# Performance work log

Measured on AMD Instinct MI355X. Metric: run time of the kernel, lower is better.

The kernel has to match this reference:

```python
import jax, jax.numpy as jnp
import numpy as np

N = 256  # n_neurons
S = 32   # state_dim
M = 32   # message_dim
E = 32   # edge_dim
B = 64   # batch
N_IN = 16

def setup_inputs() -> dict:
    key = jax.random.key(0)
    ks = jax.random.split(key, 12)
    sc = 0.1
    return {
        "inputs": jax.random.normal(ks[0], (B, N_IN, S), jnp.float32),
        "initial_state": jax.random.normal(ks[1], (N, S), jnp.float32) * sc,
        "edge_matrix": jax.random.normal(ks[2], (N, N, E), jnp.float32) * sc,
        "Wf": jax.random.normal(ks[3], (E, M * S), jnp.float32) * sc,
        "bf": jnp.zeros((M * S,), jnp.float32),
        "Wz": jax.random.normal(ks[4], (M, S), jnp.float32) * sc,
        "Uz": jax.random.normal(ks[5], (S, S), jnp.float32) * sc,
        "bz": jnp.zeros((S,), jnp.float32),
        "Wr": jax.random.normal(ks[6], (M, S), jnp.float32) * sc,
        "Ur": jax.random.normal(ks[7], (S, S), jnp.float32) * sc,
        "br": jnp.zeros((S,), jnp.float32),
        "Wh": jax.random.normal(ks[8], (M, S), jnp.float32) * sc,
        "Uh": jax.random.normal(ks[9], (S, S), jnp.float32) * sc,
        "bh": jnp.zeros((S,), jnp.float32),
        "n_outputs": 16,
    }

def reference(inputs, initial_state, edge_matrix, Wf, bf, Wz, Uz, bz, Wr, Ur, br, Wh, Uh, bh, n_outputs):
    b, n_in, s = inputs.shape
    n = initial_state.shape[0]
    # filter generation: [N,N,E] -> [N,N,M,S]
    filters = (edge_matrix @ Wf + bf).reshape(n, n, M, s)
    # init + scatter inputs into hidden state (neuron i <- inputs[:, i, :])
    h = jnp.tile(initial_state[None], (b, 1, 1)).at[:, :n_in, :].set(inputs)
    # dense edge-filtered message passing: messages[b,j,m] = sum_i filters[i,j,m,s] h[b,i,s]
    messages = jnp.einsum('bis,ijms->bjm', h, filters)
    # GRU update with message as input
    z = jax.nn.sigmoid(messages @ Wz + h @ Uz + bz)
    r = jax.nn.sigmoid(messages @ Wr + h @ Ur + br)
    h_tilde = jnp.tanh(messages @ Wh + (r * h) @ Uh + bh)
    h_new = (1.0 - z) * h + z * h_tilde
    # gather outputs from the last n_outputs neurons (reversed), permute to [n_out, B, S]
    out_idx = n - 1 - jnp.arange(n_outputs)
    outputs = jnp.transpose(h_new[:, out_idx, :], (1, 0, 2))
    return (outputs, h_new)
```

## Files before the change

### kernel.cpp

```cpp
#include <hip/hip_runtime.h>

typedef unsigned short u16;
typedef __attribute__((ext_vector_type(4))) unsigned short u16x4;
typedef __attribute__((ext_vector_type(8))) unsigned short u16x8;
typedef __attribute__((ext_vector_type(4))) float f32x4;


__device__ __forceinline__ u16 f2bf(float x){
  unsigned u = __builtin_bit_cast(unsigned, x);
  u += 0x7FFFu + ((u >> 16) & 1u);
  return (u16)(u >> 16);
}
__device__ __forceinline__ void mfma1616(f32x4& acc, u16x8 a, u16x8 b){
  asm volatile("v_mfma_f32_16x16x32_bf16 %0, %1, %2, %0" : "+v"(acc) : "v"(a), "v"(b));
}
__device__ __forceinline__ void gl16(const void* g, void* l){
  __builtin_amdgcn_global_load_lds((const __attribute__((address_space(1))) void*)g,
                                   (__attribute__((address_space(3))) void*)l, 16, 0, 0);
}
__device__ __forceinline__ float sigm(float x){ return 1.f/(1.f + __expf(-x)); }
__device__ __forceinline__ float tanh_f(float x){ return 1.f - 2.f/(1.f + __expf(2.f*x)); }

__global__ __launch_bounds__(256) void k_prep(const float* __restrict__ inputs, const float* __restrict__ init,
    const float* __restrict__ EM, const float* __restrict__ Wf, const float* __restrict__ bfv,
    const float* __restrict__ Wz, const float* __restrict__ Uz, const float* __restrict__ Wr,
    const float* __restrict__ Ur, const float* __restrict__ Wh, const float* __restrict__ Uh,
    u16* __restrict__ hT, u16* __restrict__ EMT, u16* __restrict__ Wf5,
    float* __restrict__ bterm, u16* __restrict__ wsT){
  __shared__ float tl[64*65];
  const int bid = blockIdx.x, t = threadIdx.x;
  if (bid < 512){
    int bx = bid & 127, by = bid >> 7;
    int i0 = by*64, c0 = bx*64;
#pragma unroll
    for (int p=0;p<4;++p){
      int ri = p*16 + (t>>4), c4 = (t&15)*4;
      f32x4 v = *(const f32x4*)(EM + (i0+ri)*8192 + c0 + c4);
#pragma unroll
      for (int q=0;q<4;++q) tl[ri*65 + c4 + q] = v[q];
    }
    __syncthreads();
#pragma unroll
    for (int p=0;p<4;++p){
      int rc = p*16 + (t>>4), i4 = (t&15)*4;
      u16x4 o;
#pragma unroll
      for (int q=0;q<4;++q) o[q] = f2bf(tl[(i4+q)*65 + rc]);
      *(u16x4*)(EMT + (c0+rc)*256 + i0 + i4) = o;
    }
  } else if (bid < 1024){
    int base = ((bid-512)*256 + t)*4;
    int r = base >> 8, i0 = base & 255;
    int b = r >> 5, s = r & 31;
    u16x4 v;
#pragma unroll
    for (int q=0;q<4;++q){
      int i = i0 + q;
      float x = (i < 16) ? inputs[(b*16 + i)*32 + s] : init[i*32 + s];
      v[q] = f2bf(x);
    }
    *(u16x4*)(hT + base) = v;
  } else if (bid < 1056){
    int o = ((bid-1024)*256 + t)*4;
    int m = o >> 10, rem = o & 1023, s = rem >> 5, e0 = rem & 31;
    u16x4 v;
#pragma unroll
    for (int q=0;q<4;++q) v[q] = f2bf(Wf[(e0+q)*1024 + m*32 + s]);
    *(u16x4*)(Wf5 + o) = v;
  } else if (bid < 1120){
    int b = bid - 1056;
    float* red = tl;
    float* hsum = tl + 256;
    int g = t >> 5, s = t & 31;
    float acc = 0.f;
    for (int c=0;c<32;++c){
      int i = c*8 + g;
      acc += (i < 16) ? inputs[(b*16 + i)*32 + s] : init[i*32 + s];
    }
    red[g*32 + s] = acc;
    __syncthreads();
    if (t < 32){
      float v = 0.f;
#pragma unroll
      for (int gg=0;gg<8;++gg) v += red[gg*32 + t];
      hsum[t] = v;
    }
    __syncthreads();
    if (t < 32){
      float v = 0.f;
      for (int s2=0;s2<32;++s2) v += hsum[s2] * bfv[t*32 + s2];
      bterm[b*32 + t] = v;
    }
  } else {
    const float* Ws[6] = {Wz,Uz,Wr,Ur,Wh,Uh};
    for (int idx = t; idx < 6144; idx += 256){
      int g = idx >> 10, r2 = idx & 1023, s = r2 >> 5, k = r2 & 31;
      wsT[g*1024 + s*32 + k] = f2bf(Ws[g][k*32 + s]);
    }
  }
}

__global__ __launch_bounds__(256, 3) void k_mega(const u16* __restrict__ hT, const u16* __restrict__ EMT,
    const u16* __restrict__ Wf5, const float* __restrict__ bterm, const u16* __restrict__ wsT,
    const float* __restrict__ inputs, const float* __restrict__ init,
    const float* __restrict__ bz, const float* __restrict__ br, const float* __restrict__ bh,
    float* __restrict__ out){
  __shared__ char smem[48128];
  const int t = threadIdx.x, w = t >> 6, l = t & 63;
  const int rb = blockIdx.x & 15, cb = blockIdx.x >> 4;
  const int r0 = rb*128, c0 = cb*128;
  const int wrow = (w >> 1)*64, wcol = (w & 1)*64;

  f32x4 acc[4][4];
#pragma unroll
  for (int i=0;i<4;++i)
#pragma unroll
    for (int j=0;j<4;++j)
#pragma unroll
      for (int q=0;q<4;++q) acc[i][j][q] = 0.f;

  for (int st=0; st<4; ++st){
    const int kk = st*64;
#pragma unroll
    for (int p=0;p<4;++p){
      int q = p*256 + t, r = q>>3, sl = q&7;
      gl16(hT + (r0 + r)*256 + kk + ((sl ^ (r&7))*8), smem + q*16);
    }
#pragma unroll
    for (int p=0;p<4;++p){
      int q = p*256 + t, c = q>>3, sl = q&7;
      gl16(EMT + (c0 + c)*256 + kk + ((sl ^ (c&7))*8), smem + 16384 + q*16);
    }
    __syncthreads();
#pragma unroll
    for (int ks=0; ks<2; ++ks){
      const int kg = ks*4 + (l>>4);
      u16x8 af[4], bfr[4];
#pragma unroll
      for (int mf=0; mf<4; ++mf){
        int row = wrow + mf*16 + (l&15);
        af[mf] = *(const u16x8*)(smem + row*128 + ((kg ^ (row&7))<<4));
      }
#pragma unroll
      for (int nf=0; nf<4; ++nf){
        int col = wcol + nf*16 + (l&15);
        bfr[nf] = *(const u16x8*)(smem + 16384 + col*128 + ((kg ^ (col&7))<<4));
      }
#pragma unroll
      for (int mf=0; mf<4; ++mf)
#pragma unroll
        for (int nf=0; nf<4; ++nf)
          mfma1616(acc[mf][nf], af[mf], bfr[nf]);
    }
    __syncthreads();
  }

#pragma unroll
  for (int mf=0;mf<4;++mf)
#pragma unroll
    for (int nf=0;nf<4;++nf){
      int colg = wcol + nf*16 + (l&15);
#pragma unroll
      for (int q=0;q<4;++q){
        int rowg = wrow + mf*16 + (l>>4)*4 + q;
        *(u16*)(smem + rowg*256 + ((colg*2) ^ ((rowg&7)<<4))) = f2bf(acc[mf][nf][q]);
      }
    }
  __syncthreads();

  f32x4 ea0, ea1;
#pragma unroll
  for (int q=0;q<4;++q){ ea0[q]=0.f; ea1[q]=0.f; }
  {
    const int colbj = l & 15;
    const int bloc = colbj >> 2, jloc = colbj & 3;
    const int eg = (l >> 4)*8;
#pragma unroll
    for (int ss=0; ss<8; ++ss){
      int s = w*8 + ss;
      int row = bloc*32 + s;
      u16x8 bfr = *(const u16x8*)(smem + row*256 + ((jloc*64 + eg*2) ^ ((row&7)<<4)));
      u16x8 af0 = *(const u16x8*)(Wf5 + colbj*1024 + s*32 + eg);
      u16x8 af1 = *(const u16x8*)(Wf5 + (16+colbj)*1024 + s*32 + eg);
      mfma1616(ea0, af0, bfr);
      mfma1616(ea1, af1, bfr);
    }
  }
  float* red = (float*)(smem + 32768);
  *(f32x4*)(red + ((w*2+0)*64 + l)*4) = ea0;
  *(f32x4*)(red + ((w*2+1)*64 + l)*4) = ea1;
  __syncthreads();

  float* Lmsg = (float*)(smem + 40960);
  u16*   Lmsgb = (u16*)(smem + 43008);
  float* Lh   = (float*)(smem + 44032);
  u16*   Lhb  = (u16*)(smem + 46080);
  u16*   Lrh  = (u16*)(smem + 47104);
  for (int o = t; o < 512; o += 256){
    int row = o >> 5, m = o & 31;
    int hh = m >> 4, mloc = m & 15;
    int lsrc = row | ((mloc >> 2) << 4);
    int q = mloc & 3;
    float sum = 0.f;
#pragma unroll
    for (int wv=0; wv<4; ++wv) sum += red[((wv*2+hh)*64 + lsrc)*4 + q];
    int bg = rb*4 + (row>>2), jg = cb*4 + (row&3);
    float mval = sum + bterm[bg*32 + m];
    Lmsg[row*32+m] = mval; Lmsgb[row*32+m] = f2bf(mval);
    float hval = (jg < 16) ? inputs[(bg*16 + jg)*32 + m] : init[jg*32 + m];
    Lh[row*32+m] = hval; Lhb[row*32+m] = f2bf(hval);
  }
  __syncthreads();

  if (w == 0){
    const int rloc = l & 15;
    const int kg8 = (l >> 4)*8;
    u16x8 am = *(const u16x8*)(Lmsgb + rloc*32 + kg8);
    u16x8 ah = *(const u16x8*)(Lhb   + rloc*32 + kg8);
    u16x8 wz0 = *(const u16x8*)(wsT + 0*1024 + rloc*32 + kg8);
    u16x8 wz1 = *(const u16x8*)(wsT + 0*1024 + (16+rloc)*32 + kg8);
    u16x8 uz0 = *(const u16x8*)(wsT + 1*1024 + rloc*32 + kg8);
    u16x8 uz1 = *(const u16x8*)(wsT + 1*1024 + (16+rloc)*32 + kg8);
    u16x8 wr0 = *(const u16x8*)(wsT + 2*1024 + rloc*32 + kg8);
    u16x8 wr1 = *(const u16x8*)(wsT + 2*1024 + (16+rloc)*32 + kg8);
    u16x8 ur0 = *(const u16x8*)(wsT + 3*1024 + rloc*32 + kg8);
    u16x8 ur1 = *(const u16x8*)(wsT + 3*1024 + (16+rloc)*32 + kg8);
    u16x8 wh0 = *(const u16x8*)(wsT + 4*1024 + rloc*32 + kg8);
    u16x8 wh1 = *(const u16x8*)(wsT + 4*1024 + (16+rloc)*32 + kg8);
    u16x8 uh0 = *(const u16x8*)(wsT + 5*1024 + rloc*32 + kg8);
    u16x8 uh1 = *(const u16x8*)(wsT + 5*1024 + (16+rloc)*32 + kg8);
    f32x4 zp0,zp1,rp0,rp1,hp0,hp1;
#pragma unroll
    for (int q=0;q<4;++q){ zp0[q]=0;zp1[q]=0;rp0[q]=0;rp1[q]=0;hp0[q]=0;hp1[q]=0; }
    mfma1616(zp0, am, wz0); mfma1616(zp0, ah, uz0);
    mfma1616(zp1, am, wz1); mfma1616(zp1, ah, uz1);
    mfma1616(rp0, am, wr0); mfma1616(rp0, ah, ur0);
    mfma1616(rp1, am, wr1); mfma1616(rp1, ah, ur1);
    mfma1616(hp0, am, wh0);
    mfma1616(hp1, am, wh1);
    const int crow = (l>>4)*4, cs = l & 15;
    float bz0 = bz[cs], bz1 = bz[16+cs], br0 = br[cs], br1 = br[16+cs];
    f32x4 z0,z1;
#pragma unroll
    for (int q=0;q<4;++q){
      z0[q] = sigm(zp0[q]+bz0); z1[q] = sigm(zp1[q]+bz1);
      float r0 = sigm(rp0[q]+br0), r1 = sigm(rp1[q]+br1);
      Lrh[(crow+q)*32 + cs]    = f2bf(r0 * Lh[(crow+q)*32 + cs]);
      Lrh[(crow+q)*32 + 16+cs] = f2bf(r1 * Lh[(crow+q)*32 + 16+cs]);
    }
    u16x8 arh = *(const u16x8*)(Lrh + rloc*32 + kg8);
    mfma1616(hp0, arh, uh0);
    mfma1616(hp1, arh, uh1);
    float bh0 = bh[cs], bh1 = bh[16+cs];
#pragma unroll
    for (int q=0;q<4;++q){
      int rw = crow + q;
      float ht0 = tanh_f(hp0[q]+bh0), ht1 = tanh_f(hp1[q]+bh1);
      float h0 = Lh[rw*32+cs], h1 = Lh[rw*32+16+cs];
      float hn0 = (1.f - z0[q])*h0 + z0[q]*ht0;
      float hn1 = (1.f - z1[q])*h1 + z1[q]*ht1;
      int bg = rb*4 + (rw>>2), jg = cb*4 + (rw&3);
      int base = 32768 + (bg*256 + jg)*32;
      out[base + cs] = hn0; out[base + 16 + cs] = hn1;
      if (jg >= 240){
        int ob = (255-jg)*2048 + bg*32;
        out[ob + cs] = hn0; out[ob + 16 + cs] = hn1;
      }
    }
  }
}

extern "C" void kernel_launch(void* const* d_in, const int* in_sizes, int n_in,
                              void* d_out, int out_size, void* d_ws, size_t ws_size,
                              hipStream_t stream) {
  const float* inputs = (const float*)d_in[0];
  const float* init   = (const float*)d_in[1];
  const float* EM     = (const float*)d_in[2];
  const float* Wf     = (const float*)d_in[3];
  const float* bfv    = (const float*)d_in[4];
  const float* Wz     = (const float*)d_in[5];
  const float* Uz     = (const float*)d_in[6];
  const float* bz     = (const float*)d_in[7];
  const float* Wr     = (const float*)d_in[8];
  const float* Ur     = (const float*)d_in[9];
  const float* br     = (const float*)d_in[10];
  const float* Wh     = (const float*)d_in[11];
  const float* Uh     = (const float*)d_in[12];
  const float* bh     = (const float*)d_in[13];
  float* out = (float*)d_out;
  char* ws = (char*)d_ws;

  u16* hT      = (u16*)ws;
  u16* EMT     = (u16*)(ws + (1u<<20));
  u16* Wf5     = (u16*)(ws + (5u<<20));
  float* bterm = (float*)(ws + (5u<<20) + 65536);
  u16* wsT     = (u16*)(ws + (5u<<20) + 65536 + 8192);

  k_prep<<<1121, 256, 0, stream>>>(inputs, init, EM, Wf, bfv, Wz, Uz, Wr, Ur, Wh, Uh,
                                   hT, EMT, Wf5, bterm, wsT);
  k_mega<<<1024, 256, 0, stream>>>(hT, EMT, Wf5, bterm, wsT, inputs, init, bz, br, bh, out);
}
```

Before: 121.1 us.

## Double-buffer GEMM k-loop with smaller stages and raise occupancy to four blocks

The main GEMM loop now uses 32-wide k stages with double-buffered LDS loads, so the next stage's global-to-LDS copy is issued while the current stage's MFMAs run. The shared buffer shrinks to 40 KB and launch bounds rise to 4 blocks per CU to allow more concurrency. Block indices are remapped to change how tiles are spread across the hardware, and the GRU weight loads are scoped so fewer registers are live at once. The risks are register pressure from the higher occupancy target and extra barriers from the shorter k stages.

```diff
diff --git a/kernel.cpp b/kernel.cpp
--- a/kernel.cpp
+++ b/kernel.cpp
@@ -100,14 +100,15 @@
   }
 }
 
-__global__ __launch_bounds__(256, 3) void k_mega(const u16* __restrict__ hT, const u16* __restrict__ EMT,
+__global__ __launch_bounds__(256, 4) void k_mega(const u16* __restrict__ hT, const u16* __restrict__ EMT,
     const u16* __restrict__ Wf5, const float* __restrict__ bterm, const u16* __restrict__ wsT,
     const float* __restrict__ inputs, const float* __restrict__ init,
     const float* __restrict__ bz, const float* __restrict__ br, const float* __restrict__ bh,
     float* __restrict__ out){
-  __shared__ char smem[48128];
+  __shared__ char smem[40960];
   const int t = threadIdx.x, w = t >> 6, l = t & 63;
-  const int rb = blockIdx.x & 15, cb = blockIdx.x >> 4;
+  const int logical = (blockIdx.x & 7)*128 + (blockIdx.x >> 3);
+  const int rb = logical & 15, cb = logical >> 4;
   const int r0 = rb*128, c0 = cb*128;
   const int wrow = (w >> 1)*64, wcol = (w & 1)*64;
 
@@ -119,41 +120,44 @@
 #pragma unroll
       for (int q=0;q<4;++q) acc[i][j][q] = 0.f;
 
-  for (int st=0; st<4; ++st){
-    const int kk = st*64;
-#pragma unroll
-    for (int p=0;p<4;++p){
-      int q = p*256 + t, r = q>>3, sl = q&7;
-      gl16(hT + (r0 + r)*256 + kk + ((sl ^ (r&7))*8), smem + q*16);
-    }
-#pragma unroll
-    for (int p=0;p<4;++p){
-      int q = p*256 + t, c = q>>3, sl = q&7;
-      gl16(EMT + (c0 + c)*256 + kk + ((sl ^ (c&7))*8), smem + 16384 + q*16);
+#define STAGE(st, p) do { \
+    const u16* gA = hT + r0*256 + (st)*32; \
+    const u16* gB = EMT + c0*256 + (st)*32; \
+    char* ba_ = smem + (p)*16384; \
+    _Pragma("unroll") \
+    for (int pp=0; pp<2; ++pp){ \
+      int q = pp*256 + t; \
+      int row_ = q >> 2, u_ = q & 3; \
+      int src = row_*256 + ((u_ ^ ((row_>>1)&3))*8); \
+      gl16(gA + src, ba_ + q*16); \
+      gl16(gB + src, ba_ + 8192 + q*16); \
+    } \
+  } while(0)
+
+  STAGE(0, 0);
+  __syncthreads();
+  const int lrow = l & 15;
+  const int slot = ((l>>4) ^ ((lrow>>1)&3)) << 4;
+#pragma unroll
+  for (int st=0; st<8; ++st){
+    if (st < 7) STAGE(st+1, (st+1)&1);
+    const char* ba = smem + (st&1)*16384;
+    u16x8 af[4];
+#pragma unroll
+    for (int mf=0; mf<4; ++mf){
+      int row = wrow + mf*16 + lrow;
+      af[mf] = *(const u16x8*)(ba + row*64 + slot);
+    }
+#pragma unroll
+    for (int nf=0; nf<4; ++nf){
+      int col = wcol + nf*16 + lrow;
+      u16x8 bfr = *(const u16x8*)(ba + 8192 + col*64 + slot);
+#pragma unroll
+      for (int mf=0; mf<4; ++mf) mfma1616(acc[mf][nf], af[mf], bfr);
     }
     __syncthreads();
-#pragma unroll
-    for (int ks=0; ks<2; ++ks){
-      const int kg = ks*4 + (l>>4);
-      u16x8 af[4], bfr[4];
-#pragma unroll
-      for (int mf=0; mf<4; ++mf){
-        int row = wrow + mf*16 + (l&15);
-        af[mf] = *(const u16x8*)(smem + row*128 + ((kg ^ (row&7))<<4));
-      }
-#pragma unroll
-      for (int nf=0; nf<4; ++nf){
-        int col = wcol + nf*16 + (l&15);
-        bfr[nf] = *(const u16x8*)(smem + 16384 + col*128 + ((kg ^ (col&7))<<4));
-      }
-#pragma unroll
-      for (int mf=0; mf<4; ++mf)
-#pragma unroll
-        for (int nf=0; nf<4; ++nf)
-          mfma1616(acc[mf][nf], af[mf], bfr[nf]);
-    }
-    __syncthreads();
-  }
+  }
+#undef STAGE
 
 #pragma unroll
   for (int mf=0;mf<4;++mf)
@@ -191,11 +195,11 @@
   *(f32x4*)(red + ((w*2+1)*64 + l)*4) = ea1;
   __syncthreads();
 
-  float* Lmsg = (float*)(smem + 40960);
-  u16*   Lmsgb = (u16*)(smem + 43008);
-  float* Lh   = (float*)(smem + 44032);
-  u16*   Lhb  = (u16*)(smem + 46080);
-  u16*   Lrh  = (u16*)(smem + 47104);
+  float* Lmsg  = (float*)(smem);
+  u16*   Lmsgb = (u16*)(smem + 2048);
+  float* Lh    = (float*)(smem + 3072);
+  u16*   Lhb   = (u16*)(smem + 5120);
+  u16*   Lrh   = (u16*)(smem + 6144);
   for (int o = t; o < 512; o += 256){
     int row = o >> 5, m = o & 31;
     int hh = m >> 4, mloc = m & 15;
@@ -217,27 +221,31 @@
     const int kg8 = (l >> 4)*8;
     u16x8 am = *(const u16x8*)(Lmsgb + rloc*32 + kg8);
     u16x8 ah = *(const u16x8*)(Lhb   + rloc*32 + kg8);
-    u16x8 wz0 = *(const u16x8*)(wsT + 0*1024 + rloc*32 + kg8);
-    u16x8 wz1 = *(const u16x8*)(wsT + 0*1024 + (16+rloc)*32 + kg8);
-    u16x8 uz0 = *(const u16x8*)(wsT + 1*1024 + rloc*32 + kg8);
-    u16x8 uz1 = *(const u16x8*)(wsT + 1*1024 + (16+rloc)*32 + kg8);
-    u16x8 wr0 = *(const u16x8*)(wsT + 2*1024 + rloc*32 + kg8);
-    u16x8 wr1 = *(const u16x8*)(wsT + 2*1024 + (16+rloc)*32 + kg8);
-    u16x8 ur0 = *(const u16x8*)(wsT + 3*1024 + rloc*32 + kg8);
-    u16x8 ur1 = *(const u16x8*)(wsT + 3*1024 + (16+rloc)*32 + kg8);
-    u16x8 wh0 = *(const u16x8*)(wsT + 4*1024 + rloc*32 + kg8);
-    u16x8 wh1 = *(const u16x8*)(wsT + 4*1024 + (16+rloc)*32 + kg8);
-    u16x8 uh0 = *(const u16x8*)(wsT + 5*1024 + rloc*32 + kg8);
-    u16x8 uh1 = *(const u16x8*)(wsT + 5*1024 + (16+rloc)*32 + kg8);
     f32x4 zp0,zp1,rp0,rp1,hp0,hp1;
 #pragma unroll
     for (int q=0;q<4;++q){ zp0[q]=0;zp1[q]=0;rp0[q]=0;rp1[q]=0;hp0[q]=0;hp1[q]=0; }
-    mfma1616(zp0, am, wz0); mfma1616(zp0, ah, uz0);
-    mfma1616(zp1, am, wz1); mfma1616(zp1, ah, uz1);
-    mfma1616(rp0, am, wr0); mfma1616(rp0, ah, ur0);
-    mfma1616(rp1, am, wr1); mfma1616(rp1, ah, ur1);
-    mfma1616(hp0, am, wh0);
-    mfma1616(hp1, am, wh1);
+    {
+      u16x8 wz0 = *(const u16x8*)(wsT + 0*1024 + rloc*32 + kg8);
+      u16x8 wz1 = *(const u16x8*)(wsT + 0*1024 + (16+rloc)*32 + kg8);
+      u16x8 uz0 = *(const u16x8*)(wsT + 1*1024 + rloc*32 + kg8);
+      u16x8 uz1 = *(const u16x8*)(wsT + 1*1024 + (16+rloc)*32 + kg8);
+      mfma1616(zp0, am, wz0); mfma1616(zp0, ah, uz0);
+      mfma1616(zp1, am, wz1); mfma1616(zp1, ah, uz1);
+    }
+    {
+      u16x8 wr0 = *(const u16x8*)(wsT + 2*1024 + rloc*32 + kg8);
+      u16x8 wr1 = *(const u16x8*)(wsT + 2*1024 + (16+rloc)*32 + kg8);
+      u16x8 ur0 = *(const u16x8*)(wsT + 3*1024 + rloc*32 + kg8);
+      u16x8 ur1 = *(const u16x8*)(wsT + 3*1024 + (16+rloc)*32 + kg8);
+      mfma1616(rp0, am, wr0); mfma1616(rp0, ah, ur0);
+      mfma1616(rp1, am, wr1); mfma1616(rp1, ah, ur1);
+    }
+    {
+      u16x8 wh0 = *(const u16x8*)(wsT + 4*1024 + rloc*32 + kg8);
+      u16x8 wh1 = *(const u16x8*)(wsT + 4*1024 + (16+rloc)*32 + kg8);
+      mfma1616(hp0, am, wh0);
+      mfma1616(hp1, am, wh1);
+    }
     const int crow = (l>>4)*4, cs = l & 15;
     float bz0 = bz[cs], bz1 = bz[16+cs], br0 = br[cs], br1 = br[16+cs];
     f32x4 z0,z1;
@@ -249,8 +257,12 @@
       Lrh[(crow+q)*32 + 16+cs] = f2bf(r1 * Lh[(crow+q)*32 + 16+cs]);
     }
     u16x8 arh = *(const u16x8*)(Lrh + rloc*32 + kg8);
-    mfma1616(hp0, arh, uh0);
-    mfma1616(hp1, arh, uh1);
+    {
+      u16x8 uh0 = *(const u16x8*)(wsT + 5*1024 + rloc*32 + kg8);
+      u16x8 uh1 = *(const u16x8*)(wsT + 5*1024 + (16+rloc)*32 + kg8);
+      mfma1616(hp0, arh, uh0);
+      mfma1616(hp1, arh, uh1);
+    }
     float bh0 = bh[cs], bh1 = bh[16+cs];
 #pragma unroll
     for (int q=0;q<4;++q){
```

New measurement: 114.3 us. 5.6% less time.
